# Kernel optimization log

Measured on AMD Instinct MI355X. Metric: run time of the kernel, lower is better.

## Reference

```python
import jax, jax.numpy as jnp
import numpy as np
import math

B, C, IMG, P = 32, 3, 224, 16
E, DEPTH, H, MLP = 768, 12, 12, 3072
NP = (IMG // P) ** 2          # 196 patches
S = NP + 1                    # 197 tokens with cls
NCLS = 10
HD = E // H                   # 64 head dim
EPS = 1e-5


def setup_inputs() -> dict:
    key = jax.random.key(0)
    ks = iter(jax.random.split(key, 64))
    n = lambda shape, s=0.02: (jax.random.normal(next(ks), shape, jnp.float32) * s)
    inp = {
        "x": jax.random.normal(next(ks), (B, C, IMG, IMG), jnp.float32),
        "conv_w": n((E, C, P, P)),
        "conv_b": jnp.zeros((E,), jnp.float32),
        "cls_token": n((1, 1, E)),
        "pos_embed": n((1, S, E)),
        # stacked per-layer params, leading dim DEPTH; linear weights stored [in, out]
        "ln1_w": jnp.ones((DEPTH, E), jnp.float32),
        "ln1_b": jnp.zeros((DEPTH, E), jnp.float32),
        "qkv_w": n((DEPTH, E, 3 * E)),
        "qkv_b": jnp.zeros((DEPTH, 3 * E), jnp.float32),
        "proj_w": n((DEPTH, E, E)),
        "proj_b": jnp.zeros((DEPTH, E), jnp.float32),
        "ln2_w": jnp.ones((DEPTH, E), jnp.float32),
        "ln2_b": jnp.zeros((DEPTH, E), jnp.float32),
        "mlp_w1": n((DEPTH, E, MLP)),
        "mlp_b1": jnp.zeros((DEPTH, MLP), jnp.float32),
        "mlp_w2": n((DEPTH, MLP, E)),
        "mlp_b2": jnp.zeros((DEPTH, E), jnp.float32),
        "lnf_w": jnp.ones((E,), jnp.float32),
        "lnf_b": jnp.zeros((E,), jnp.float32),
        "head_w": n((E, NCLS)),
        "head_b": jnp.zeros((NCLS,), jnp.float32),
    }
    return inp


def layernorm(x, w, b):
    mu = jnp.mean(x, axis=-1, keepdims=True)
    var = jnp.mean(jnp.square(x - mu), axis=-1, keepdims=True)
    return (x - mu) * jax.lax.rsqrt(var + EPS) * w + b


def reference(x, conv_w, conv_b, cls_token, pos_embed,
              ln1_w, ln1_b, qkv_w, qkv_b, proj_w, proj_b,
              ln2_w, ln2_b, mlp_w1, mlp_b1, mlp_w2, mlp_b2,
              lnf_w, lnf_b, head_w, head_b):
    # --- patch embedding: stride-P, kernel-P conv == patchify + matmul ---
    g = IMG // P  # 14
    patches = x.reshape(B, C, g, P, g, P).transpose(0, 2, 4, 1, 3, 5).reshape(B, NP, C * P * P)
    wp = conv_w.reshape(E, C * P * P)
    tok = jnp.einsum('bpd,ed->bpe', patches, wp) + conv_b  # [B, NP, E]

    # cls token + positional embedding (dropout = identity at eval)
    h = jnp.concatenate([jnp.broadcast_to(cls_token, (B, 1, E)), tok], axis=1) + pos_embed

    scale = math.sqrt(HD)
    for i in range(DEPTH):
        # --- attention ---
        y = layernorm(h, ln1_w[i], ln1_b[i])
        qkv = (y @ qkv_w[i] + qkv_b[i]).reshape(B, S, 3, H, HD)
        q, k, v = qkv[:, :, 0], qkv[:, :, 1], qkv[:, :, 2]  # [B, S, H, HD]
        attn = jnp.einsum('bqhd,bkhd->bhqk', q, k) / scale
        attn = jax.nn.softmax(attn, axis=-1)
        o = jnp.einsum('bhqk,bkhd->bqhd', attn, v).reshape(B, S, E)
        h = h + (o @ proj_w[i] + proj_b[i])
        # --- MLP ---
        y = layernorm(h, ln2_w[i], ln2_b[i])
        y = jax.nn.gelu(y @ mlp_w1[i] + mlp_b1[i], approximate=False)
        h = h + (y @ mlp_w2[i] + mlp_b2[i])

    h = layernorm(h, lnf_w, lnf_b)
    return h[:, 0] @ head_w + head_b  # [B, NCLS]
```

## Files before the change

### kernel.cpp

```cpp
#include <hip/hip_runtime.h>


typedef __attribute__((ext_vector_type(8))) short short8;
typedef __attribute__((ext_vector_type(8))) unsigned short ushort8;
typedef __attribute__((ext_vector_type(4))) float f32x4;
typedef unsigned short u16;

#define DEV __device__ __forceinline__

DEV u16 f2bf(float f) {
  unsigned int u = __builtin_bit_cast(unsigned int, f);
  u += 0x7fffu + ((u >> 16) & 1u);
  return (u16)(u >> 16);
}
DEV float wred_sum(float v) {
  for (int o = 32; o; o >>= 1) v += __shfl_xor(v, o, 64);
  return v;
}
DEV void glds16(const void* gp, void* lp) {
  __builtin_amdgcn_global_load_lds(
      (const __attribute__((address_space(1))) void*)gp,
      (__attribute__((address_space(3))) void*)lp, 16, 0, 0);
}
DEV int xcd_swz(int flat, int nwg) {
  int q = nwg >> 3, r = nwg & 7;
  int x = flat & 7, o = flat >> 3;
  return (x < r ? x * (q + 1) : r * (q + 1) + (x - r) * q) + o;
}

__global__ __launch_bounds__(256) void cvt4_k(const float* __restrict__ s,
                                              u16* __restrict__ d, long n4) {
  long i = (long)blockIdx.x * 256 + threadIdx.x;
  if (i >= n4) return;
  float4 v = ((const float4*)s)[i];
  ushort4 o;
  o.x = f2bf(v.x); o.y = f2bf(v.y); o.z = f2bf(v.z); o.w = f2bf(v.w);
  ((ushort4*)d)[i] = o;
}

__global__ __launch_bounds__(256) void tpose_k(const float* __restrict__ s,
                                               u16* __restrict__ d, int K,
                                               int N) {
  __shared__ float t[32][33];
  const int bx = blockIdx.x;
  const int by = blockIdx.y;
  const size_t base = (size_t)blockIdx.z * K * N;
  const int c = threadIdx.x & 31, r0 = threadIdx.x >> 5;
#pragma unroll
  for (int i = 0; i < 4; ++i) {
    int r = r0 + i * 8;
    t[r][c] = s[base + (size_t)(by * 32 + r) * N + bx * 32 + c];
  }
  __syncthreads();
#pragma unroll
  for (int i = 0; i < 4; ++i) {
    int r = r0 + i * 8;
    d[base + (size_t)(bx * 32 + r) * K + by * 32 + c] = f2bf(t[c][r]);
  }
}

__global__ __launch_bounds__(256) void patch_k(const float* __restrict__ x,
                                               u16* __restrict__ pt) {
  int i = blockIdx.x * 256 + threadIdx.x;
  int d = i % 768;
  int bp = i / 768;
  int p = bp % 196, b = bp / 196;
  int c = d >> 8, pd = d & 255;
  int py = pd >> 4, px = pd & 15;
  int gy = p / 14, gx = p - gy * 14;
  size_t src = ((size_t)(b * 3 + c) * 224 + gy * 16 + py) * 224 + gx * 16 + px;
  pt[i] = f2bf(x[src]);
}

__global__ __launch_bounds__(256) void clspos_k(const float* __restrict__ cls,
                                                const float* __restrict__ pos,
                                                float* __restrict__ h) {
  int i = blockIdx.x * 256 + threadIdx.x;
  int b = i / 768, e = i - b * 768;
  h[(size_t)b * 197 * 768 + e] = cls[e] + pos[e];
}

template <int EPI>
DEV void epi_store(float v, int grow, int gcol, u16* outb, int ldo,
                   float* outf, const float* pos) {
  if constexpr (EPI == 0) {
    outb[(size_t)grow * ldo + gcol] = f2bf(v);
  } else if constexpr (EPI == 1) {
    float u = __expf(-1.5957691216f * (v + 0.044715f * v * v * v));
    outb[(size_t)grow * ldo + gcol] = f2bf(v / (1.f + u));
  } else if constexpr (EPI == 2) {
    outf[(size_t)grow * ldo + gcol] += v;
  } else {
    int b = grow / 196, p = grow - b * 196;
    outf[(size_t)(grow + b + 1) * 768 + gcol] =
        v + pos[(size_t)(p + 1) * 768 + gcol];
  }
}

template <int EPI>
__global__ __launch_bounds__(512) void gemmK64(
    const u16* __restrict__ A, int lda, const u16* __restrict__ Bt, int ldb,
    const float* __restrict__ bias, u16* __restrict__ outb, int ldo,
    float* __restrict__ outf, const float* __restrict__ pos, int M, int N,
    int K) {
  __shared__ __align__(16) u16 Ak[2][128 * 64];
  __shared__ __align__(16) u16 Bk[2][128 * 64];
  const int tid = threadIdx.x;
  const int lane = tid & 63, wid = tid >> 6;
  const int wm = wid >> 2, wn = wid & 3;
  const int lg = lane >> 4, lr = lane & 15;
  const int nwg = gridDim.x * gridDim.y;
  const int wg = xcd_swz(blockIdx.y * gridDim.x + blockIdx.x, nwg);
  const int tn = wg % gridDim.x, tm = wg / gridDim.x;

  const int r8 = lane >> 3, c8 = lane & 7;
  const int swc = (c8 ^ r8) << 3;
  const u16* aS = A + (size_t)(tm * 128 + wid * 16 + r8) * lda + swc;
  const u16* bS = Bt + (size_t)(tn * 128 + wid * 16 + r8) * ldb + swc;

  auto stage = [&](int buf, int kt) {
    const u16* ak = aS + kt * 64;
    const u16* bk = bS + kt * 64;
    u16* ad = &Ak[buf][wid * 1024];
    u16* bd = &Bk[buf][wid * 1024];
    glds16(ak, ad);
    glds16(ak + (size_t)8 * lda, ad + 512);
    glds16(bk, bd);
    glds16(bk + (size_t)8 * ldb, bd + 512);
  };

  f32x4 acc[4][2] = {};
  auto compute = [&](int buf) {
#pragma unroll
    for (int ks = 0; ks < 2; ++ks) {
      const int pc = (ks << 2) | lg;
      const int po = ((pc ^ (lr & 7)) << 3);
      short8 af[4], bf2[2];
#pragma unroll
      for (int i = 0; i < 4; ++i)
        af[i] = *(const short8*)(&Ak[buf][(wm * 64 + i * 16 + lr) * 64 + po]);
#pragma unroll
      for (int i = 0; i < 2; ++i)
        bf2[i] = *(const short8*)(&Bk[buf][(wn * 32 + i * 16 + lr) * 64 + po]);
#pragma unroll
      for (int mi = 0; mi < 4; ++mi)
#pragma unroll
        for (int ni = 0; ni < 2; ++ni)
          acc[mi][ni] = __builtin_amdgcn_mfma_f32_16x16x32_bf16(
              af[mi], bf2[ni], acc[mi][ni], 0, 0, 0);
    }
  };

  const int nk = K >> 6;
  int cur = 0;
  stage(0, 0);
  __syncthreads();
  for (int kt = 0; kt < nk - 1; ++kt) {
    stage(cur ^ 1, kt + 1);
    compute(cur);
    __syncthreads();
    cur ^= 1;
  }
  compute(cur);

#pragma unroll
  for (int mi = 0; mi < 4; ++mi)
#pragma unroll
    for (int ni = 0; ni < 2; ++ni)
#pragma unroll
      for (int r = 0; r < 4; ++r) {
        int grow = tm * 128 + wm * 64 + mi * 16 + lg * 4 + r;
        int gcol = tn * 128 + wn * 32 + ni * 16 + lr;
        if (grow < M)
          epi_store<EPI>(acc[mi][ni][r] + bias[gcol], grow, gcol, outb, ldo,
                         outf, pos);
      }
}

template <int EPI, int BM>
__global__ __launch_bounds__(256) void gemmP(
    const u16* __restrict__ A, int lda, const u16* __restrict__ Bt, int ldb,
    const float* __restrict__ bias, u16* __restrict__ outb, int ldo,
    float* __restrict__ outf, const float* __restrict__ pos, int M, int N,
    int K) {
  constexpr int MI = BM / 32;
  __shared__ __align__(16) u16 Ak[2][BM * 32];
  __shared__ __align__(16) u16 Bk[2][128 * 32];
  const int tid = threadIdx.x;
  const int lane = tid & 63, wid = tid >> 6;
  const int wm = wid >> 1, wn = wid & 1;
  const int lg = lane >> 4, lr = lane & 15;
  const int nwg = gridDim.x * gridDim.y;
  const int wg = xcd_swz(blockIdx.y * gridDim.x + blockIdx.x, nwg);
  const int tn = wg % gridDim.x, tm = wg / gridDim.x;

  const int sr = lane >> 2;
  const int sc4 = (((lane & 3) ^ ((lane >> 3) & 3)) << 3);
  const u16* aSrc = A + (size_t)(tm * BM + wid * (BM / 4) + sr) * lda + sc4;
  const u16* bSrc = Bt + (size_t)(tn * 128 + wid * 32 + sr) * ldb + sc4;
  const size_t aRow16 = (size_t)16 * lda, bRow16 = (size_t)16 * ldb;

  auto stage = [&](int buf, int kt) {
    const u16* ak = aSrc + kt * 32;
    const u16* bk = bSrc + kt * 32;
    u16* ad = &Ak[buf][wid * (BM / 4) * 32];
    u16* bd = &Bk[buf][wid * 1024];
    glds16(ak, ad);
    if constexpr (BM == 128) glds16(ak + aRow16, ad + 512);
    glds16(bk, bd);
    glds16(bk + bRow16, bd + 512);
  };

  const int rp = (lg ^ ((lr >> 1) & 3)) << 3;
  f32x4 acc[MI][4] = {};
  auto compute = [&](int buf) {
    short8 af[MI], bfr[4];
#pragma unroll
    for (int i = 0; i < MI; ++i)
      af[i] =
          *(const short8*)(&Ak[buf][(wm * (BM / 2) + i * 16 + lr) * 32 + rp]);
#pragma unroll
    for (int i = 0; i < 4; ++i)
      bfr[i] = *(const short8*)(&Bk[buf][(wn * 64 + i * 16 + lr) * 32 + rp]);
#pragma unroll
    for (int mi = 0; mi < MI; ++mi)
#pragma unroll
      for (int ni = 0; ni < 4; ++ni)
        acc[mi][ni] = __builtin_amdgcn_mfma_f32_16x16x32_bf16(
            af[mi], bfr[ni], acc[mi][ni], 0, 0, 0);
  };

  const int nk = K >> 5;
  int cur = 0;
  stage(0, 0);
  __syncthreads();
  for (int kt = 0; kt < nk - 1; ++kt) {
    stage(cur ^ 1, kt + 1);
    compute(cur);
    __syncthreads();
    cur ^= 1;
  }
  compute(cur);

#pragma unroll
  for (int mi = 0; mi < MI; ++mi)
#pragma unroll
    for (int ni = 0; ni < 4; ++ni)
#pragma unroll
      for (int r = 0; r < 4; ++r) {
        int grow = tm * BM + wm * (BM / 2) + mi * 16 + lg * 4 + r;
        int gcol = tn * 128 + wn * 64 + ni * 16 + lr;
        if (grow < M)
          epi_store<EPI>(acc[mi][ni][r] + bias[gcol], grow, gcol, outb, ldo,
                         outf, pos);
      }
}

__global__ __launch_bounds__(64) void qksm_k(const u16* __restrict__ qkv,
                                             u16* __restrict__ P) {
  const int bh = blockIdx.x;
  const int qt = blockIdx.y;
  const int lane = threadIdx.x;
  const int lg = lane >> 4, lr = lane & 15;
  const int b = bh / 12, hh = bh - b * 12;
  const u16* base = qkv + (size_t)b * 197 * 2304 + hh * 64;
  int qrow = qt * 16 + lr;
  if (qrow > 196) qrow = 196;
  const u16* qp = base + (size_t)qrow * 2304 + lg * 8;
  short8 a0 = *(const short8*)(qp);
  short8 a1 = *(const short8*)(qp + 32);
  f32x4 c[13];
  const bool kval[2] = {true, (12 * 16 + lr) <= 196};
#pragma unroll
  for (int kt = 0; kt < 13; ++kt) {
    int krow = kt * 16 + lr;
    if (krow > 196) krow = 196;
    const u16* kp = base + 768 + (size_t)krow * 2304 + lg * 8;
    short8 b0 = *(const short8*)(kp);
    short8 b1 = *(const short8*)(kp + 32);
    f32x4 t = {0.f, 0.f, 0.f, 0.f};
    t = __builtin_amdgcn_mfma_f32_16x16x32_bf16(a0, b0, t, 0, 0, 0);
    c[kt] = __builtin_amdgcn_mfma_f32_16x16x32_bf16(a1, b1, t, 0, 0, 0);
  }
  float mr[4], sr_[4];
#pragma unroll
  for (int r = 0; r < 4; ++r) {
    float mm = -3.4e38f;
#pragma unroll
    for (int kt = 0; kt < 13; ++kt)
      if (kval[kt == 12]) mm = fmaxf(mm, c[kt][r] * 0.125f);
#pragma unroll
    for (int o = 1; o < 16; o <<= 1) mm = fmaxf(mm, __shfl_xor(mm, o, 64));
    mr[r] = mm;
  }
#pragma unroll
  for (int r = 0; r < 4; ++r) {
    float s = 0.f;
#pragma unroll
    for (int kt = 0; kt < 13; ++kt) {
      float e = kval[kt == 12] ? __expf(c[kt][r] * 0.125f - mr[r]) : 0.f;
      c[kt][r] = e;
      s += e;
    }
#pragma unroll
    for (int o = 1; o < 16; o <<= 1) s += __shfl_xor(s, o, 64);
    sr_[r] = 1.0f / s;
  }
  u16* pb = P + (size_t)bh * 197 * 224;
#pragma unroll
  for (int r = 0; r < 4; ++r) {
    int q = qt * 16 + lg * 4 + r;
    if (q < 197) {
#pragma unroll
      for (int kt = 0; kt < 13; ++kt)
        pb[(size_t)q * 224 + kt * 16 + lr] = f2bf(c[kt][r] * sr_[r]);
      pb[(size_t)q * 224 + 208 + lr] = 0;
    }
  }
}

__global__ __launch_bounds__(256) void pv_k(const u16* __restrict__ qkv,
                                            const u16* __restrict__ P,
                                            u16* __restrict__ o) {
  const int bh = blockIdx.x;
  const int b = bh / 12, hh = bh - b * 12;
  const int tid = threadIdx.x;
  const int lane = tid & 63, ct = tid >> 6;
  const int lg = lane >> 4, lr = lane & 15;
  const u16* vbase =
      qkv + (size_t)b * 197 * 2304 + 1536 + hh * 64 + ct * 16 + lr;
  short8 vf[7];
#pragma unroll
  for (int ks = 0; ks < 7; ++ks) {
    ushort8 t;
#pragma unroll
    for (int j = 0; j < 8; ++j) {
      int kk = ks * 32 + lg * 8 + j;
      if (kk > 196) kk = 196;
      t[j] = vbase[(size_t)kk * 2304];
    }
    vf[ks] = __builtin_bit_cast(short8, t);
  }
  const u16* pbase = P + (size_t)bh * 197 * 224;
  u16* ob = o + (size_t)b * 197 * 768 + hh * 64 + ct * 16;
  for (int qt = 0; qt < 13; ++qt) {
    int q = qt * 16 + lr;
    if (q > 196) q = 196;
    const u16* pp = pbase + (size_t)q * 224 + lg * 8;
    f32x4 acc = {0.f, 0.f, 0.f, 0.f};
#pragma unroll
    for (int ks = 0; ks < 7; ++ks) {
      short8 af = *(const short8*)(pp + ks * 32);
      acc = __builtin_amdgcn_mfma_f32_16x16x32_bf16(af, vf[ks], acc, 0, 0, 0);
    }
#pragma unroll
    for (int r = 0; r < 4; ++r) {
      int qq = qt * 16 + lg * 4 + r;
      if (qq < 197) ob[(size_t)qq * 768 + lr] = f2bf(acc[r]);
    }
  }
}

__global__ __launch_bounds__(256) void ln_k(const float* __restrict__ x,
                                            const float* __restrict__ w,
                                            const float* __restrict__ bb,
                                            u16* __restrict__ y) {
  const int r = blockIdx.x, tid = threadIdx.x;
  const float* xr = x + (size_t)r * 768;
  float v0 = xr[tid], v1 = xr[tid + 256], v2 = xr[tid + 512];
  float s = v0 + v1 + v2;
  float q = v0 * v0 + v1 * v1 + v2 * v2;
  s = wred_sum(s);
  q = wred_sum(q);
  __shared__ float ss[4], qs[4];
  int lane = tid & 63, wid = tid >> 6;
  if (lane == 0) { ss[wid] = s; qs[wid] = q; }
  __syncthreads();
  float S = ss[0] + ss[1] + ss[2] + ss[3];
  float Q = qs[0] + qs[1] + qs[2] + qs[3];
  float mu = S * (1.f / 768.f);
  float var = Q * (1.f / 768.f) - mu * mu;
  float rs = rsqrtf(var + 1e-5f);
  u16* yr = y + (size_t)r * 768;
  yr[tid] = f2bf((v0 - mu) * rs * w[tid] + bb[tid]);
  yr[tid + 256] = f2bf((v1 - mu) * rs * w[tid + 256] + bb[tid + 256]);
  yr[tid + 512] = f2bf((v2 - mu) * rs * w[tid + 512] + bb[tid + 512]);
}

__global__ __launch_bounds__(256) void head_k(
    const float* __restrict__ h, const float* __restrict__ lnw,
    const float* __restrict__ lnb, const float* __restrict__ hw,
    const float* __restrict__ hb, float* __restrict__ out) {
  const int b = blockIdx.x, tid = threadIdx.x;
  const float* xr = h + (size_t)b * 197 * 768;
  float v0 = xr[tid], v1 = xr[tid + 256], v2 = xr[tid + 512];
  float s = v0 + v1 + v2;
  float q = v0 * v0 + v1 * v1 + v2 * v2;
  s = wred_sum(s);
  q = wred_sum(q);
  __shared__ float ss[4], qs[4];
  int lane = tid & 63, wid = tid >> 6;
  if (lane == 0) { ss[wid] = s; qs[wid] = q; }
  __syncthreads();
  float S = ss[0] + ss[1] + ss[2] + ss[3];
  float Q = qs[0] + qs[1] + qs[2] + qs[3];
  float mu = S * (1.f / 768.f);
  float var = Q * (1.f / 768.f) - mu * mu;
  float rs = rsqrtf(var + 1e-5f);
  __shared__ float yb[768];
  yb[tid] = (v0 - mu) * rs * lnw[tid] + lnb[tid];
  yb[tid + 256] = (v1 - mu) * rs * lnw[tid + 256] + lnb[tid + 256];
  yb[tid + 512] = (v2 - mu) * rs * lnw[tid + 512] + lnb[tid + 512];
  __syncthreads();
  float p[10] = {};
  for (int e = tid; e < 768; e += 256) {
    float yv = yb[e];
#pragma unroll
    for (int n = 0; n < 10; ++n) p[n] += yv * hw[(size_t)e * 10 + n];
  }
#pragma unroll
  for (int n = 0; n < 10; ++n) p[n] = wred_sum(p[n]);
  __shared__ float red[4][10];
  if (lane == 0)
#pragma unroll
    for (int n = 0; n < 10; ++n) red[wid][n] = p[n];
  __syncthreads();
  if (tid < 10)
    out[b * 10 + tid] =
        red[0][tid] + red[1][tid] + red[2][tid] + red[3][tid] + hb[tid];
}

extern "C" void kernel_launch(void* const* d_in, const int* in_sizes, int n_in,
                              void* d_out, int out_size, void* d_ws,
                              size_t ws_size, hipStream_t stream) {
  const float* x = (const float*)d_in[0];
  const float* conv_w = (const float*)d_in[1];
  const float* conv_b = (const float*)d_in[2];
  const float* cls = (const float*)d_in[3];
  const float* pos = (const float*)d_in[4];
  const float* ln1w = (const float*)d_in[5];
  const float* ln1b = (const float*)d_in[6];
  const float* qkvw = (const float*)d_in[7];
  const float* qkvbias = (const float*)d_in[8];
  const float* projw = (const float*)d_in[9];
  const float* projb = (const float*)d_in[10];
  const float* ln2w = (const float*)d_in[11];
  const float* ln2b = (const float*)d_in[12];
  const float* w1f = (const float*)d_in[13];
  const float* b1 = (const float*)d_in[14];
  const float* w2f = (const float*)d_in[15];
  const float* b2 = (const float*)d_in[16];
  const float* lnfw = (const float*)d_in[17];
  const float* lnfb = (const float*)d_in[18];
  const float* headw = (const float*)d_in[19];
  const float* headb = (const float*)d_in[20];
  float* out = (float*)d_out;

  char* p = (char*)d_ws;
  auto take = [&](size_t bytes) {
    char* q = p;
    p += (bytes + 255) & ~(size_t)255;
    return q;
  };
  u16* wq = (u16*)take(12ull * 768 * 2304 * 2);
  u16* wpj = (u16*)take(12ull * 768 * 768 * 2);
  u16* w1 = (u16*)take(12ull * 768 * 3072 * 2);
  u16* w2 = (u16*)take(12ull * 3072 * 768 * 2);
  u16* wc = (u16*)take(768ull * 768 * 2);
  float* h = (float*)take(6304ull * 768 * 4);
  u16* y = (u16*)take(6400ull * 768 * 2);
  u16* qkv = (u16*)take(6400ull * 2304 * 2);
  u16* ob = (u16*)take(6400ull * 768 * 2);
  u16* mlpb = (u16*)take(6400ull * 3072 * 2);
  u16* P = (u16*)take(384ull * 197 * 224 * 2);
  (void)ws_size; (void)in_sizes; (void)n_in; (void)out_size;

  tpose_k<<<dim3(72, 24, 12), 256, 0, stream>>>(qkvw, wq, 768, 2304);
  tpose_k<<<dim3(24, 24, 12), 256, 0, stream>>>(projw, wpj, 768, 768);
  tpose_k<<<dim3(96, 24, 12), 256, 0, stream>>>(w1f, w1, 768, 3072);
  tpose_k<<<dim3(24, 96, 12), 256, 0, stream>>>(w2f, w2, 3072, 768);
  cvt4_k<<<576, 256, 0, stream>>>(conv_w, wc, 768 * 768 / 4);

  patch_k<<<6272 * 768 / 256, 256, 0, stream>>>(x, mlpb);
  gemmP<3, 64><<<dim3(6, 98), 256, 0, stream>>>(mlpb, 768, wc, 768, conv_b,
                                                nullptr, 0, h, pos, 6272, 768,
                                                768);
  clspos_k<<<32 * 768 / 256, 256, 0, stream>>>(cls, pos, h);

  for (int i = 0; i < 12; ++i) {
    ln_k<<<6304, 256, 0, stream>>>(h, ln1w + i * 768, ln1b + i * 768, y);
    gemmK64<0><<<dim3(18, 50), 512, 0, stream>>>(
        y, 768, wq + (size_t)i * 768 * 2304, 768, qkvbias + i * 2304, qkv,
        2304, nullptr, nullptr, 6304, 2304, 768);
    qksm_k<<<dim3(384, 13), 64, 0, stream>>>(qkv, P);
    pv_k<<<384, 256, 0, stream>>>(qkv, P, ob);
    gemmP<2, 64><<<dim3(6, 99), 256, 0, stream>>>(
        ob, 768, wpj + (size_t)i * 768 * 768, 768, projb + i * 768, nullptr,
        768, h, nullptr, 6304, 768, 768);
    ln_k<<<6304, 256, 0, stream>>>(h, ln2w + i * 768, ln2b + i * 768, y);
    gemmK64<1><<<dim3(24, 50), 512, 0, stream>>>(
        y, 768, w1 + (size_t)i * 768 * 3072, 768, b1 + i * 3072, mlpb, 3072,
        nullptr, nullptr, 6304, 3072, 768);
    gemmP<2, 64><<<dim3(6, 99), 256, 0, stream>>>(
        mlpb, 3072, w2 + (size_t)i * 3072 * 768, 3072, b2 + i * 768, nullptr,
        768, h, nullptr, 6304, 768, 3072);
  }

  head_k<<<32, 256, 0, stream>>>(h, lnfw, lnfb, headw, headb, out);
}
```

Measured before the change: 3.223 ms.

## Use 32-row tiles with BK=64 for N=768 GEMMs; one-wave-per-row layernorm

The N=768 GEMMs (patch embed, attention projection, MLP down) swap the 64x128 tile with BK=32 for a 32x128 tile with BK=64 and an XOR-swizzled LDS layout. This doubles the workgroup count, so the 256 CUs are better filled for these small-N shapes, and halves the number of K-loop barriers. The cost is less operand reuse per tile and more total global traffic for B. LayerNorm now uses one wave per row with float4 loads and no shared-memory reduction, which cuts block-level sync and launch overhead.

Result: slower. 3.395 ms (+5.3%).

```diff
diff --git a/kernel.cpp b/kernel.cpp
--- a/kernel.cpp
+++ b/kernel.cpp
@@ -177,60 +177,60 @@
       }
 }
 
-template <int EPI, int BM>
-__global__ __launch_bounds__(256) void gemmP(
+template <int EPI>
+__global__ __launch_bounds__(256) void gemmS(
     const u16* __restrict__ A, int lda, const u16* __restrict__ Bt, int ldb,
     const float* __restrict__ bias, u16* __restrict__ outb, int ldo,
     float* __restrict__ outf, const float* __restrict__ pos, int M, int N,
     int K) {
-  constexpr int MI = BM / 32;
-  __shared__ __align__(16) u16 Ak[2][BM * 32];
-  __shared__ __align__(16) u16 Bk[2][128 * 32];
+  __shared__ __align__(16) u16 Ak[2][32 * 64];
+  __shared__ __align__(16) u16 Bk[2][128 * 64];
   const int tid = threadIdx.x;
   const int lane = tid & 63, wid = tid >> 6;
-  const int wm = wid >> 1, wn = wid & 1;
   const int lg = lane >> 4, lr = lane & 15;
   const int nwg = gridDim.x * gridDim.y;
   const int wg = xcd_swz(blockIdx.y * gridDim.x + blockIdx.x, nwg);
   const int tn = wg % gridDim.x, tm = wg / gridDim.x;
 
-  const int sr = lane >> 2;
-  const int sc4 = (((lane & 3) ^ ((lane >> 3) & 3)) << 3);
-  const u16* aSrc = A + (size_t)(tm * BM + wid * (BM / 4) + sr) * lda + sc4;
-  const u16* bSrc = Bt + (size_t)(tn * 128 + wid * 32 + sr) * ldb + sc4;
-  const size_t aRow16 = (size_t)16 * lda, bRow16 = (size_t)16 * ldb;
+  const int r8 = lane >> 3, c8 = lane & 7;
+  const int swc = (c8 ^ r8) << 3;
+  const u16* aS = A + (size_t)(tm * 32 + wid * 8 + r8) * lda + swc;
+  const u16* bS = Bt + (size_t)(tn * 128 + wid * 32 + r8) * ldb + swc;
 
   auto stage = [&](int buf, int kt) {
-    const u16* ak = aSrc + kt * 32;
-    const u16* bk = bSrc + kt * 32;
-    u16* ad = &Ak[buf][wid * (BM / 4) * 32];
-    u16* bd = &Bk[buf][wid * 1024];
-    glds16(ak, ad);
-    if constexpr (BM == 128) glds16(ak + aRow16, ad + 512);
-    glds16(bk, bd);
-    glds16(bk + bRow16, bd + 512);
+    const u16* ak = aS + kt * 64;
+    const u16* bk = bS + kt * 64;
+    glds16(ak, &Ak[buf][wid * 512]);
+    u16* bd = &Bk[buf][wid * 2048];
+#pragma unroll
+    for (int c = 0; c < 4; ++c)
+      glds16(bk + (size_t)(c * 8) * ldb, bd + c * 512);
   };
 
-  const int rp = (lg ^ ((lr >> 1) & 3)) << 3;
-  f32x4 acc[MI][4] = {};
+  f32x4 acc[2][2] = {};
   auto compute = [&](int buf) {
-    short8 af[MI], bfr[4];
-#pragma unroll
-    for (int i = 0; i < MI; ++i)
-      af[i] =
-          *(const short8*)(&Ak[buf][(wm * (BM / 2) + i * 16 + lr) * 32 + rp]);
-#pragma unroll
-    for (int i = 0; i < 4; ++i)
-      bfr[i] = *(const short8*)(&Bk[buf][(wn * 64 + i * 16 + lr) * 32 + rp]);
-#pragma unroll
-    for (int mi = 0; mi < MI; ++mi)
-#pragma unroll
-      for (int ni = 0; ni < 4; ++ni)
-        acc[mi][ni] = __builtin_amdgcn_mfma_f32_16x16x32_bf16(
-            af[mi], bfr[ni], acc[mi][ni], 0, 0, 0);
+#pragma unroll
+    for (int ks = 0; ks < 2; ++ks) {
+      const int pc = (ks << 2) | lg;
+      const int po = ((pc ^ (lr & 7)) << 3);
+      short8 af[2], bf2[2];
+#pragma unroll
+      for (int i = 0; i < 2; ++i)
+        af[i] = *(const short8*)(&Ak[buf][(i * 16 + lr) * 64 + po]);
+#pragma unroll
+      for (int i = 0; i < 2; ++i)
+        bf2[i] =
+            *(const short8*)(&Bk[buf][(wid * 32 + i * 16 + lr) * 64 + po]);
+#pragma unroll
+      for (int mi = 0; mi < 2; ++mi)
+#pragma unroll
+        for (int ni = 0; ni < 2; ++ni)
+          acc[mi][ni] = __builtin_amdgcn_mfma_f32_16x16x32_bf16(
+              af[mi], bf2[ni], acc[mi][ni], 0, 0, 0);
+    }
   };
 
-  const int nk = K >> 5;
+  const int nk = K >> 6;
   int cur = 0;
   stage(0, 0);
   __syncthreads();
@@ -243,13 +243,13 @@
   compute(cur);
 
 #pragma unroll
-  for (int mi = 0; mi < MI; ++mi)
-#pragma unroll
-    for (int ni = 0; ni < 4; ++ni)
+  for (int mi = 0; mi < 2; ++mi)
+#pragma unroll
+    for (int ni = 0; ni < 2; ++ni)
 #pragma unroll
       for (int r = 0; r < 4; ++r) {
-        int grow = tm * BM + wm * (BM / 2) + mi * 16 + lg * 4 + r;
-        int gcol = tn * 128 + wn * 64 + ni * 16 + lr;
+        int grow = tm * 32 + mi * 16 + lg * 4 + r;
+        int gcol = tn * 128 + wid * 32 + ni * 16 + lr;
         if (grow < M)
           epi_store<EPI>(acc[mi][ni][r] + bias[gcol], grow, gcol, outb, ldo,
                          outf, pos);
@@ -365,26 +365,35 @@
                                             const float* __restrict__ w,
                                             const float* __restrict__ bb,
                                             u16* __restrict__ y) {
-  const int r = blockIdx.x, tid = threadIdx.x;
+  const int lane = threadIdx.x & 63, wv = threadIdx.x >> 6;
+  const int r = blockIdx.x * 4 + wv;
   const float* xr = x + (size_t)r * 768;
-  float v0 = xr[tid], v1 = xr[tid + 256], v2 = xr[tid + 512];
-  float s = v0 + v1 + v2;
-  float q = v0 * v0 + v1 * v1 + v2 * v2;
+  float4 v[3];
+  float s = 0.f, q = 0.f;
+#pragma unroll
+  for (int i = 0; i < 3; ++i) {
+    v[i] = *(const float4*)(xr + i * 256 + lane * 4);
+    s += v[i].x + v[i].y + v[i].z + v[i].w;
+    q += v[i].x * v[i].x + v[i].y * v[i].y + v[i].z * v[i].z +
+         v[i].w * v[i].w;
+  }
   s = wred_sum(s);
   q = wred_sum(q);
-  __shared__ float ss[4], qs[4];
-  int lane = tid & 63, wid = tid >> 6;
-  if (lane == 0) { ss[wid] = s; qs[wid] = q; }
-  __syncthreads();
-  float S = ss[0] + ss[1] + ss[2] + ss[3];
-  float Q = qs[0] + qs[1] + qs[2] + qs[3];
-  float mu = S * (1.f / 768.f);
-  float var = Q * (1.f / 768.f) - mu * mu;
+  float mu = s * (1.f / 768.f);
+  float var = q * (1.f / 768.f) - mu * mu;
   float rs = rsqrtf(var + 1e-5f);
   u16* yr = y + (size_t)r * 768;
-  yr[tid] = f2bf((v0 - mu) * rs * w[tid] + bb[tid]);
-  yr[tid + 256] = f2bf((v1 - mu) * rs * w[tid + 256] + bb[tid + 256]);
-  yr[tid + 512] = f2bf((v2 - mu) * rs * w[tid + 512] + bb[tid + 512]);
+#pragma unroll
+  for (int i = 0; i < 3; ++i) {
+    float4 wv4 = *(const float4*)(w + i * 256 + lane * 4);
+    float4 bv4 = *(const float4*)(bb + i * 256 + lane * 4);
+    ushort4 o;
+    o.x = f2bf((v[i].x - mu) * rs * wv4.x + bv4.x);
+    o.y = f2bf((v[i].y - mu) * rs * wv4.y + bv4.y);
+    o.z = f2bf((v[i].z - mu) * rs * wv4.z + bv4.z);
+    o.w = f2bf((v[i].w - mu) * rs * wv4.w + bv4.w);
+    *(ushort4*)(yr + i * 256 + lane * 4) = o;
+  }
 }
 
 __global__ __launch_bounds__(256) void head_k(
@@ -482,26 +491,26 @@
   cvt4_k<<<576, 256, 0, stream>>>(conv_w, wc, 768 * 768 / 4);
 
   patch_k<<<6272 * 768 / 256, 256, 0, stream>>>(x, mlpb);
-  gemmP<3, 64><<<dim3(6, 98), 256, 0, stream>>>(mlpb, 768, wc, 768, conv_b,
-                                                nullptr, 0, h, pos, 6272, 768,
-                                                768);
+  gemmS<3><<<dim3(6, 196), 256, 0, stream>>>(mlpb, 768, wc, 768, conv_b,
+                                             nullptr, 0, h, pos, 6272, 768,
+                                             768);
   clspos_k<<<32 * 768 / 256, 256, 0, stream>>>(cls, pos, h);
 
   for (int i = 0; i < 12; ++i) {
-    ln_k<<<6304, 256, 0, stream>>>(h, ln1w + i * 768, ln1b + i * 768, y);
+    ln_k<<<1576, 256, 0, stream>>>(h, ln1w + i * 768, ln1b + i * 768, y);
     gemmK64<0><<<dim3(18, 50), 512, 0, stream>>>(
         y, 768, wq + (size_t)i * 768 * 2304, 768, qkvbias + i * 2304, qkv,
         2304, nullptr, nullptr, 6304, 2304, 768);
     qksm_k<<<dim3(384, 13), 64, 0, stream>>>(qkv, P);
     pv_k<<<384, 256, 0, stream>>>(qkv, P, ob);
-    gemmP<2, 64><<<dim3(6, 99), 256, 0, stream>>>(
+    gemmS<2><<<dim3(6, 197), 256, 0, stream>>>(
         ob, 768, wpj + (size_t)i * 768 * 768, 768, projb + i * 768, nullptr,
         768, h, nullptr, 6304, 768, 768);
-    ln_k<<<6304, 256, 0, stream>>>(h, ln2w + i * 768, ln2b + i * 768, y);
+    ln_k<<<1576, 256, 0, stream>>>(h, ln2w + i * 768, ln2b + i * 768, y);
     gemmK64<1><<<dim3(24, 50), 512, 0, stream>>>(
         y, 768, w1 + (size_t)i * 768 * 3072, 768, b1 + i * 3072, mlpb, 3072,
         nullptr, nullptr, 6304, 3072, 768);
-    gemmP<2, 64><<<dim3(6, 99), 256, 0, stream>>>(
+    gemmS<2><<<dim3(6, 197), 256, 0, stream>>>(
         mlpb, 3072, w2 + (size_t)i * 3072 * 768, 3072, b2 + i * 768, nullptr,
         768, h, nullptr, 6304, 768, 3072);
   }
```

## Split-K the MLP down-projection with 128x128 tiles and vectorize layernorm

Applied to the files above, without the earlier changes.

Replaces the 64-row-tile MLP second GEMM with a two-way split-K kernel using 128x128 tiles and 512 threads. Each split writes fp32 partials into the dead y/qkv workspace, and a separate reduction kernel adds both partials, the bias and the residual into h. This aims to raise per-block data reuse and MFMA density, at the cost of an extra fp32 partial round-trip through memory and one more launch. Layernorm is also rewritten to process one row per wavefront with float4 loads and packed bf16 stores, which drops the shared-memory reduction and the block barrier.

New measurement: 3.135 ms. 2.7% less time.

```diff
diff --git a/kernel.cpp b/kernel.cpp
--- a/kernel.cpp
+++ b/kernel.cpp
@@ -175,6 +175,100 @@
           epi_store<EPI>(acc[mi][ni][r] + bias[gcol], grow, gcol, outb, ldo,
                          outf, pos);
       }
+}
+
+__global__ __launch_bounds__(512) void gemmSK(const u16* __restrict__ A,
+                                              int lda,
+                                              const u16* __restrict__ Bt,
+                                              int ldb, float* __restrict__ Cp,
+                                              int M, int KC) {
+  __shared__ __align__(16) u16 Ak[2][128 * 64];
+  __shared__ __align__(16) u16 Bk[2][128 * 64];
+  const int tid = threadIdx.x;
+  const int lane = tid & 63, wid = tid >> 6;
+  const int wm = wid >> 2, wn = wid & 3;
+  const int lg = lane >> 4, lr = lane & 15;
+  const int z = blockIdx.z;
+  const int nwg = gridDim.x * gridDim.y;
+  const int wg = xcd_swz(blockIdx.y * gridDim.x + blockIdx.x, nwg);
+  const int tn = wg % gridDim.x, tm = wg / gridDim.x;
+
+  const int r8 = lane >> 3, c8 = lane & 7;
+  const int swc = (c8 ^ r8) << 3;
+  const u16* aS = A + (size_t)(tm * 128 + wid * 16 + r8) * lda + z * KC + swc;
+  const u16* bS = Bt + (size_t)(tn * 128 + wid * 16 + r8) * ldb + z * KC + swc;
+
+  auto stage = [&](int buf, int kt) {
+    const u16* ak = aS + kt * 64;
+    const u16* bk = bS + kt * 64;
+    u16* ad = &Ak[buf][wid * 1024];
+    u16* bd = &Bk[buf][wid * 1024];
+    glds16(ak, ad);
+    glds16(ak + (size_t)8 * lda, ad + 512);
+    glds16(bk, bd);
+    glds16(bk + (size_t)8 * ldb, bd + 512);
+  };
+
+  f32x4 acc[4][2] = {};
+  auto compute = [&](int buf) {
+#pragma unroll
+    for (int ks = 0; ks < 2; ++ks) {
+      const int pc = (ks << 2) | lg;
+      const int po = ((pc ^ (lr & 7)) << 3);
+      short8 af[4], bf2[2];
+#pragma unroll
+      for (int i = 0; i < 4; ++i)
+        af[i] = *(const short8*)(&Ak[buf][(wm * 64 + i * 16 + lr) * 64 + po]);
+#pragma unroll
+      for (int i = 0; i < 2; ++i)
+        bf2[i] = *(const short8*)(&Bk[buf][(wn * 32 + i * 16 + lr) * 64 + po]);
+#pragma unroll
+      for (int mi = 0; mi < 4; ++mi)
+#pragma unroll
+        for (int ni = 0; ni < 2; ++ni)
+          acc[mi][ni] = __builtin_amdgcn_mfma_f32_16x16x32_bf16(
+              af[mi], bf2[ni], acc[mi][ni], 0, 0, 0);
+    }
+  };
+
+  const int nk = KC >> 6;
+  int cur = 0;
+  stage(0, 0);
+  __syncthreads();
+  for (int kt = 0; kt < nk - 1; ++kt) {
+    stage(cur ^ 1, kt + 1);
+    compute(cur);
+    __syncthreads();
+    cur ^= 1;
+  }
+  compute(cur);
+
+  float* outp = Cp + (size_t)z * M * 768;
+#pragma unroll
+  for (int mi = 0; mi < 4; ++mi)
+#pragma unroll
+    for (int ni = 0; ni < 2; ++ni)
+#pragma unroll
+      for (int r = 0; r < 4; ++r) {
+        int grow = tm * 128 + wm * 64 + mi * 16 + lg * 4 + r;
+        int gcol = tn * 128 + wn * 32 + ni * 16 + lr;
+        if (grow < M) outp[(size_t)grow * 768 + gcol] = acc[mi][ni][r];
+      }
+}
+
+__global__ __launch_bounds__(256) void redK(const float* __restrict__ Cp,
+                                            const float* __restrict__ bias,
+                                            float* __restrict__ h) {
+  size_t i = ((size_t)blockIdx.x * 256 + threadIdx.x) * 4;
+  float4 p0 = *(const float4*)(Cp + i);
+  float4 p1 = *(const float4*)(Cp + 6304ull * 768 + i);
+  float4 hv = *(const float4*)(h + i);
+  float4 bv = *(const float4*)(bias + (int)(i % 768));
+  hv.x += p0.x + p1.x + bv.x;
+  hv.y += p0.y + p1.y + bv.y;
+  hv.z += p0.z + p1.z + bv.z;
+  hv.w += p0.w + p1.w + bv.w;
+  *(float4*)(h + i) = hv;
 }
 
 template <int EPI, int BM>
@@ -365,26 +459,35 @@
                                             const float* __restrict__ w,
                                             const float* __restrict__ bb,
                                             u16* __restrict__ y) {
-  const int r = blockIdx.x, tid = threadIdx.x;
+  const int lane = threadIdx.x & 63, wv = threadIdx.x >> 6;
+  const int r = blockIdx.x * 4 + wv;
   const float* xr = x + (size_t)r * 768;
-  float v0 = xr[tid], v1 = xr[tid + 256], v2 = xr[tid + 512];
-  float s = v0 + v1 + v2;
-  float q = v0 * v0 + v1 * v1 + v2 * v2;
+  float4 v[3];
+  float s = 0.f, q = 0.f;
+#pragma unroll
+  for (int i = 0; i < 3; ++i) {
+    v[i] = *(const float4*)(xr + i * 256 + lane * 4);
+    s += v[i].x + v[i].y + v[i].z + v[i].w;
+    q += v[i].x * v[i].x + v[i].y * v[i].y + v[i].z * v[i].z +
+         v[i].w * v[i].w;
+  }
   s = wred_sum(s);
   q = wred_sum(q);
-  __shared__ float ss[4], qs[4];
-  int lane = tid & 63, wid = tid >> 6;
-  if (lane == 0) { ss[wid] = s; qs[wid] = q; }
-  __syncthreads();
-  float S = ss[0] + ss[1] + ss[2] + ss[3];
-  float Q = qs[0] + qs[1] + qs[2] + qs[3];
-  float mu = S * (1.f / 768.f);
-  float var = Q * (1.f / 768.f) - mu * mu;
+  float mu = s * (1.f / 768.f);
+  float var = q * (1.f / 768.f) - mu * mu;
   float rs = rsqrtf(var + 1e-5f);
   u16* yr = y + (size_t)r * 768;
-  yr[tid] = f2bf((v0 - mu) * rs * w[tid] + bb[tid]);
-  yr[tid + 256] = f2bf((v1 - mu) * rs * w[tid + 256] + bb[tid + 256]);
-  yr[tid + 512] = f2bf((v2 - mu) * rs * w[tid + 512] + bb[tid + 512]);
+#pragma unroll
+  for (int i = 0; i < 3; ++i) {
+    float4 wv4 = *(const float4*)(w + i * 256 + lane * 4);
+    float4 bv4 = *(const float4*)(bb + i * 256 + lane * 4);
+    ushort4 o;
+    o.x = f2bf((v[i].x - mu) * rs * wv4.x + bv4.x);
+    o.y = f2bf((v[i].y - mu) * rs * wv4.y + bv4.y);
+    o.z = f2bf((v[i].z - mu) * rs * wv4.z + bv4.z);
+    o.w = f2bf((v[i].w - mu) * rs * wv4.w + bv4.w);
+    *(ushort4*)(yr + i * 256 + lane * 4) = o;
+  }
 }
 
 __global__ __launch_bounds__(256) void head_k(
@@ -473,6 +576,7 @@
   u16* ob = (u16*)take(6400ull * 768 * 2);
   u16* mlpb = (u16*)take(6400ull * 3072 * 2);
   u16* P = (u16*)take(384ull * 197 * 224 * 2);
+  float* skP = (float*)y;
   (void)ws_size; (void)in_sizes; (void)n_in; (void)out_size;
 
   tpose_k<<<dim3(72, 24, 12), 256, 0, stream>>>(qkvw, wq, 768, 2304);
@@ -488,7 +592,7 @@
   clspos_k<<<32 * 768 / 256, 256, 0, stream>>>(cls, pos, h);
 
   for (int i = 0; i < 12; ++i) {
-    ln_k<<<6304, 256, 0, stream>>>(h, ln1w + i * 768, ln1b + i * 768, y);
+    ln_k<<<1576, 256, 0, stream>>>(h, ln1w + i * 768, ln1b + i * 768, y);
     gemmK64<0><<<dim3(18, 50), 512, 0, stream>>>(
         y, 768, wq + (size_t)i * 768 * 2304, 768, qkvbias + i * 2304, qkv,
         2304, nullptr, nullptr, 6304, 2304, 768);
@@ -497,13 +601,13 @@
     gemmP<2, 64><<<dim3(6, 99), 256, 0, stream>>>(
         ob, 768, wpj + (size_t)i * 768 * 768, 768, projb + i * 768, nullptr,
         768, h, nullptr, 6304, 768, 768);
-    ln_k<<<6304, 256, 0, stream>>>(h, ln2w + i * 768, ln2b + i * 768, y);
+    ln_k<<<1576, 256, 0, stream>>>(h, ln2w + i * 768, ln2b + i * 768, y);
     gemmK64<1><<<dim3(24, 50), 512, 0, stream>>>(
         y, 768, w1 + (size_t)i * 768 * 3072, 768, b1 + i * 3072, mlpb, 3072,
         nullptr, nullptr, 6304, 3072, 768);
-    gemmP<2, 64><<<dim3(6, 99), 256, 0, stream>>>(
-        mlpb, 3072, w2 + (size_t)i * 3072 * 768, 3072, b2 + i * 768, nullptr,
-        768, h, nullptr, 6304, 768, 3072);
+    gemmSK<<<dim3(6, 50, 2), 512, 0, stream>>>(
+        mlpb, 3072, w2 + (size_t)i * 3072 * 768, 3072, skP, 6304, 1536);
+    redK<<<4728, 256, 0, stream>>>(skP, b2 + i * 768, h);
   }
 
   head_k<<<32, 256, 0, stream>>>(h, lnfw, lnfb, headw, headb, out);
```

## Generalize GEMM tiles, split-K for MLP down-proj, warp-per-row layernorm

Applied to the files above, without the earlier changes.

Replaces the fixed 128x128 K64 GEMM with a templated gemmU that supports 128x256 and 256x128 tiles, and uses it for the QKV, fc1 and proj GEMMs instead of the smaller-tile gemmP. The MLP down-projection becomes a two-way split-K into an fp32 scratch buffer that aliases the layernorm output buffer, followed by a reduction kernel that adds both partials, the bias and the residual. LayerNorm now gives one wavefront per row with float4 loads and no shared-memory reduction. Larger tiles improve operand reuse but cut the number of workgroups and raise register pressure. Split-K adds an extra pass over the fp32 partials.

Measured after the change: 3.556 ms. +10.3%, slower.

```diff
diff --git a/kernel.cpp b/kernel.cpp
--- a/kernel.cpp
+++ b/kernel.cpp
@@ -90,64 +90,73 @@
     outb[(size_t)grow * ldo + gcol] = f2bf(v / (1.f + u));
   } else if constexpr (EPI == 2) {
     outf[(size_t)grow * ldo + gcol] += v;
-  } else {
+  } else if constexpr (EPI == 3) {
     int b = grow / 196, p = grow - b * 196;
     outf[(size_t)(grow + b + 1) * 768 + gcol] =
         v + pos[(size_t)(p + 1) * 768 + gcol];
   }
 }
 
-template <int EPI>
-__global__ __launch_bounds__(512) void gemmK64(
+template <int EPI, int BM, int BN>
+__global__ __launch_bounds__(512) void gemmU(
     const u16* __restrict__ A, int lda, const u16* __restrict__ Bt, int ldb,
     const float* __restrict__ bias, u16* __restrict__ outb, int ldo,
-    float* __restrict__ outf, const float* __restrict__ pos, int M, int N,
-    int K) {
-  __shared__ __align__(16) u16 Ak[2][128 * 64];
-  __shared__ __align__(16) u16 Bk[2][128 * 64];
+    float* __restrict__ outf, const float* __restrict__ pos, int M, int K) {
+  constexpr int WM = BM / 64;
+  constexpr int WN = 8 / WM;
+  constexpr int WCOL = BN / WN;
+  constexpr int NI = WCOL / 16;
+  constexpr int RW = (BM + BN) / 8;
+  constexpr int NG = RW / 8;
+  __shared__ __align__(16) u16 Ak[2][BM * 64];
+  __shared__ __align__(16) u16 Bk[2][BN * 64];
   const int tid = threadIdx.x;
   const int lane = tid & 63, wid = tid >> 6;
-  const int wm = wid >> 2, wn = wid & 3;
+  const int wm = wid / WN, wn = wid % WN;
   const int lg = lane >> 4, lr = lane & 15;
   const int nwg = gridDim.x * gridDim.y;
   const int wg = xcd_swz(blockIdx.y * gridDim.x + blockIdx.x, nwg);
   const int tn = wg % gridDim.x, tm = wg / gridDim.x;
+  const size_t koff = (EPI == 4) ? (size_t)blockIdx.z * K : 0;
 
   const int r8 = lane >> 3, c8 = lane & 7;
   const int swc = (c8 ^ r8) << 3;
-  const u16* aS = A + (size_t)(tm * 128 + wid * 16 + r8) * lda + swc;
-  const u16* bS = Bt + (size_t)(tn * 128 + wid * 16 + r8) * ldb + swc;
+  const u16* aRow = A + (size_t)(tm * BM + r8) * lda + koff + swc;
+  const u16* bRow = Bt + (size_t)(tn * BN + r8) * ldb + koff + swc;
 
   auto stage = [&](int buf, int kt) {
-    const u16* ak = aS + kt * 64;
-    const u16* bk = bS + kt * 64;
-    u16* ad = &Ak[buf][wid * 1024];
-    u16* bd = &Bk[buf][wid * 1024];
-    glds16(ak, ad);
-    glds16(ak + (size_t)8 * lda, ad + 512);
-    glds16(bk, bd);
-    glds16(bk + (size_t)8 * ldb, bd + 512);
+#pragma unroll
+    for (int g = 0; g < NG; ++g) {
+      const int cr0 = wid * RW + g * 8;
+      if (cr0 < BM) {
+        glds16(aRow + (size_t)cr0 * lda + kt * 64, &Ak[buf][cr0 * 64]);
+      } else {
+        glds16(bRow + (size_t)(cr0 - BM) * ldb + kt * 64,
+               &Bk[buf][(cr0 - BM) * 64]);
+      }
+    }
   };
 
-  f32x4 acc[4][2] = {};
+  f32x4 acc[4][NI] = {};
   auto compute = [&](int buf) {
 #pragma unroll
     for (int ks = 0; ks < 2; ++ks) {
       const int pc = (ks << 2) | lg;
       const int po = ((pc ^ (lr & 7)) << 3);
-      short8 af[4], bf2[2];
+      short8 af[4], bf[NI];
 #pragma unroll
       for (int i = 0; i < 4; ++i)
         af[i] = *(const short8*)(&Ak[buf][(wm * 64 + i * 16 + lr) * 64 + po]);
 #pragma unroll
-      for (int i = 0; i < 2; ++i)
-        bf2[i] = *(const short8*)(&Bk[buf][(wn * 32 + i * 16 + lr) * 64 + po]);
+      for (int i = 0; i < NI; ++i)
+        bf[i] =
+            *(const short8*)(&Bk[buf][(wn * WCOL + i * 16 + lr) * 64 + po]);
 #pragma unroll
       for (int mi = 0; mi < 4; ++mi)
 #pragma unroll
-        for (int ni = 0; ni < 2; ++ni)
+        for (int ni = 0; ni < NI; ++ni)
           acc[mi][ni] = __builtin_amdgcn_mfma_f32_16x16x32_bf16(
-              af[mi], bf2[ni], acc[mi][ni], 0, 0, 0);
+              af[mi], bf[ni], acc[mi][ni], 0, 0, 0);
     }
   };
 
@@ -166,15 +175,36 @@
 #pragma unroll
   for (int mi = 0; mi < 4; ++mi)
 #pragma unroll
-    for (int ni = 0; ni < 2; ++ni)
+    for (int ni = 0; ni < NI; ++ni)
 #pragma unroll
       for (int r = 0; r < 4; ++r) {
-        int grow = tm * 128 + wm * 64 + mi * 16 + lg * 4 + r;
-        int gcol = tn * 128 + wn * 32 + ni * 16 + lr;
-        if (grow < M)
-          epi_store<EPI>(acc[mi][ni][r] + bias[gcol], grow, gcol, outb, ldo,
-                         outf, pos);
+        int grow = tm * BM + wm * 64 + mi * 16 + lg * 4 + r;
+        int gcol = tn * BN + wn * WCOL + ni * 16 + lr;
+        if (grow < M) {
+          float v = acc[mi][ni][r];
+          if constexpr (EPI == 4) {
+            outf[(size_t)blockIdx.z * M * ldo + (size_t)grow * ldo + gcol] =
+                v;
+          } else {
+            epi_store<EPI>(v + bias[gcol], grow, gcol, outb, ldo, outf, pos);
+          }
+        }
       }
+}
+
+__global__ __launch_bounds__(256) void redK(const float* __restrict__ Cp,
+                                            const float* __restrict__ bias,
+                                            float* __restrict__ h) {
+  size_t i = ((size_t)blockIdx.x * 256 + threadIdx.x) * 4;
+  float4 p0 = *(const float4*)(Cp + i);
+  float4 p1 = *(const float4*)(Cp + 6304ull * 768 + i);
+  float4 hv = *(const float4*)(h + i);
+  float4 bv = *(const float4*)(bias + (int)(i % 768));
+  hv.x += p0.x + p1.x + bv.x;
+  hv.y += p0.y + p1.y + bv.y;
+  hv.z += p0.z + p1.z + bv.z;
+  hv.w += p0.w + p1.w + bv.w;
+  *(float4*)(h + i) = hv;
 }
 
 template <int EPI, int BM>
@@ -365,26 +395,35 @@
                                             const float* __restrict__ w,
                                             const float* __restrict__ bb,
                                             u16* __restrict__ y) {
-  const int r = blockIdx.x, tid = threadIdx.x;
+  const int lane = threadIdx.x & 63, wv = threadIdx.x >> 6;
+  const int r = blockIdx.x * 4 + wv;
   const float* xr = x + (size_t)r * 768;
-  float v0 = xr[tid], v1 = xr[tid + 256], v2 = xr[tid + 512];
-  float s = v0 + v1 + v2;
-  float q = v0 * v0 + v1 * v1 + v2 * v2;
+  float4 v[3];
+  float s = 0.f, q = 0.f;
+#pragma unroll
+  for (int i = 0; i < 3; ++i) {
+    v[i] = *(const float4*)(xr + i * 256 + lane * 4);
+    s += v[i].x + v[i].y + v[i].z + v[i].w;
+    q += v[i].x * v[i].x + v[i].y * v[i].y + v[i].z * v[i].z +
+         v[i].w * v[i].w;
+  }
   s = wred_sum(s);
   q = wred_sum(q);
-  __shared__ float ss[4], qs[4];
-  int lane = tid & 63, wid = tid >> 6;
-  if (lane == 0) { ss[wid] = s; qs[wid] = q; }
-  __syncthreads();
-  float S = ss[0] + ss[1] + ss[2] + ss[3];
-  float Q = qs[0] + qs[1] + qs[2] + qs[3];
-  float mu = S * (1.f / 768.f);
-  float var = Q * (1.f / 768.f) - mu * mu;
+  float mu = s * (1.f / 768.f);
+  float var = q * (1.f / 768.f) - mu * mu;
   float rs = rsqrtf(var + 1e-5f);
   u16* yr = y + (size_t)r * 768;
-  yr[tid] = f2bf((v0 - mu) * rs * w[tid] + bb[tid]);
-  yr[tid + 256] = f2bf((v1 - mu) * rs * w[tid + 256] + bb[tid + 256]);
-  yr[tid + 512] = f2bf((v2 - mu) * rs * w[tid + 512] + bb[tid + 512]);
+#pragma unroll
+  for (int i = 0; i < 3; ++i) {
+    float4 wv4 = *(const float4*)(w + i * 256 + lane * 4);
+    float4 bv4 = *(const float4*)(bb + i * 256 + lane * 4);
+    ushort4 o;
+    o.x = f2bf((v[i].x - mu) * rs * wv4.x + bv4.x);
+    o.y = f2bf((v[i].y - mu) * rs * wv4.y + bv4.y);
+    o.z = f2bf((v[i].z - mu) * rs * wv4.z + bv4.z);
+    o.w = f2bf((v[i].w - mu) * rs * wv4.w + bv4.w);
+    *(ushort4*)(yr + i * 256 + lane * 4) = o;
+  }
 }
 
 __global__ __launch_bounds__(256) void head_k(
@@ -473,6 +512,7 @@
   u16* ob = (u16*)take(6400ull * 768 * 2);
   u16* mlpb = (u16*)take(6400ull * 3072 * 2);
   u16* P = (u16*)take(384ull * 197 * 224 * 2);
+  float* skP = (float*)y;
   (void)ws_size; (void)in_sizes; (void)n_in; (void)out_size;
 
   tpose_k<<<dim3(72, 24, 12), 256, 0, stream>>>(qkvw, wq, 768, 2304);
@@ -488,22 +528,23 @@
   clspos_k<<<32 * 768 / 256, 256, 0, stream>>>(cls, pos, h);
 
   for (int i = 0; i < 12; ++i) {
-    ln_k<<<6304, 256, 0, stream>>>(h, ln1w + i * 768, ln1b + i * 768, y);
-    gemmK64<0><<<dim3(18, 50), 512, 0, stream>>>(
+    ln_k<<<1576, 256, 0, stream>>>(h, ln1w + i * 768, ln1b + i * 768, y);
+    gemmU<0, 128, 256><<<dim3(9, 50), 512, 0, stream>>>(
         y, 768, wq + (size_t)i * 768 * 2304, 768, qkvbias + i * 2304, qkv,
-        2304, nullptr, nullptr, 6304, 2304, 768);
+        2304, nullptr, nullptr, 6304, 768);
     qksm_k<<<dim3(384, 13), 64, 0, stream>>>(qkv, P);
     pv_k<<<384, 256, 0, stream>>>(qkv, P, ob);
-    gemmP<2, 64><<<dim3(6, 99), 256, 0, stream>>>(
+    gemmU<2, 128, 128><<<dim3(6, 50), 512, 0, stream>>>(
         ob, 768, wpj + (size_t)i * 768 * 768, 768, projb + i * 768, nullptr,
-        768, h, nullptr, 6304, 768, 768);
-    ln_k<<<6304, 256, 0, stream>>>(h, ln2w + i * 768, ln2b + i * 768, y);
-    gemmK64<1><<<dim3(24, 50), 512, 0, stream>>>(
+        768, h, nullptr, 6304, 768);
+    ln_k<<<1576, 256, 0, stream>>>(h, ln2w + i * 768, ln2b + i * 768, y);
+    gemmU<1, 128, 256><<<dim3(12, 50), 512, 0, stream>>>(
         y, 768, w1 + (size_t)i * 768 * 3072, 768, b1 + i * 3072, mlpb, 3072,
-        nullptr, nullptr, 6304, 3072, 768);
-    gemmP<2, 64><<<dim3(6, 99), 256, 0, stream>>>(
-        mlpb, 3072, w2 + (size_t)i * 3072 * 768, 3072, b2 + i * 768, nullptr,
-        768, h, nullptr, 6304, 768, 3072);
+        nullptr, nullptr, 6304, 768);
+    gemmU<4, 256, 128><<<dim3(6, 25, 2), 512, 0, stream>>>(
+        mlpb, 3072, w2 + (size_t)i * 3072 * 768, 3072, nullptr, nullptr, 768,
+        skP, nullptr, 6304, 1536);
+    redK<<<4728, 256, 0, stream>>>(skP, b2 + i * 768, h);
   }
 
   head_k<<<32, 256, 0, stream>>>(h, lnfw, lnfb, headw, headb, out);
```
